# Kernel tuning notes

Hardware: AMD Instinct MI355X
Metric: run time of the kernel (lower is better)

Reference implementation:

```python
import jax, jax.numpy as jnp
import numpy as np

B, T, K, H = 8, 1024, 512, 8
MASKED = True

def setup_inputs() -> dict:
    key = jax.random.key(0)
    ks = jax.random.split(key, 6)
    s = 0.02
    return {
        "x": jax.random.normal(ks[0], (B, T, K), dtype=jnp.float32),
        "Wq": jax.random.normal(ks[1], (K, H * K), dtype=jnp.float32) * s,
        "Wk": jax.random.normal(ks[2], (K, H * K), dtype=jnp.float32) * s,
        "Wv": jax.random.normal(ks[3], (K, H * K), dtype=jnp.float32) * s,
        "Wu": jax.random.normal(ks[4], (H * K, K), dtype=jnp.float32) * s,
        "bu": jnp.zeros((K,), dtype=jnp.float32),
    }

def reference(x, Wq, Wk, Wv, Wu, bu):
    b, t, k = x.shape
    h = H
    scale = k ** (-0.25)  # applied to both q and k, as in the torch module
    q = (x @ Wq).reshape(b, t, h, k) * scale
    kk = (x @ Wk).reshape(b, t, h, k) * scale
    v = (x @ Wv).reshape(b, t, h, k)
    # scores: [b, h, t_q, t_k]
    dot = jnp.einsum("bthk,bshk->bhts", q, kk)
    if MASKED:
        causal = jnp.tril(jnp.ones((t, t), dtype=bool))
        dot = jnp.where(causal, dot, -jnp.inf)
    attn = jax.nn.softmax(dot, axis=-1)
    out = jnp.einsum("bhts,bshk->bthk", attn, v).reshape(b, t, h * k)
    return out @ Wu + bu
```

## Files before the change

kernel.cpp:

```cpp
#include <hip/hip_runtime.h>
#include <hip/hip_bf16.h>

#define T_SEQ 1024
#define NH 8
#define DH 512
#define HK 4096

typedef __attribute__((ext_vector_type(8))) __bf16 bf16x8;
typedef __attribute__((ext_vector_type(4))) float f32x4;

#define QK_SCALE 0.21022410381342863f
#define QK_SCALE_LOG2E 0.30328926584f

static __device__ __forceinline__ unsigned short f2bu(float f) {
  union { __hip_bfloat16 h; unsigned short u; } cv;
  cv.h = __float2bfloat16(f);
  return cv.u;
}

#define GLOAD_LDS16(gsrc, ldst) \
  __builtin_amdgcn_global_load_lds((const __attribute__((address_space(1))) void*)(gsrc), \
                                   (__attribute__((address_space(3))) void*)(ldst), 16, 0, 0)

__global__ void cvt_bf16_kernel(const float* __restrict__ in, unsigned short* __restrict__ out, int n4) {
  int i = blockIdx.x * blockDim.x + threadIdx.x;
  if (i >= n4) return;
  const float4 v = reinterpret_cast<const float4*>(in)[i];
  ushort4 u; u.x = f2bu(v.x); u.y = f2bu(v.y); u.z = f2bu(v.z); u.w = f2bu(v.w);
  reinterpret_cast<ushort4*>(out)[i] = u;
}

__global__ void transpose_cvt_kernel(const float* __restrict__ in, unsigned short* __restrict__ out,
                                     int R, int C) {
  __shared__ float tile[32][33];
  const int c0 = blockIdx.x * 32, r0 = blockIdx.y * 32;
  const int tx = threadIdx.x, ty = threadIdx.y;
  #pragma unroll
  for (int i = ty; i < 32; i += 8)
    tile[i][tx] = in[(size_t)(r0 + i) * C + (c0 + tx)];
  __syncthreads();
  #pragma unroll
  for (int i = ty; i < 32; i += 8)
    out[(size_t)(c0 + i) * R + (r0 + tx)] = f2bu(tile[tx][i]);
}

__global__ void transpose_cvt3_kernel(const float* __restrict__ Wq, const float* __restrict__ Wk,
                                      const float* __restrict__ Wv, unsigned short* __restrict__ out) {
  __shared__ float tile[32][33];
  const float* in = (blockIdx.z == 0) ? Wq : (blockIdx.z == 1) ? Wk : Wv;
  unsigned short* dst = out + (size_t)blockIdx.z * 4096 * 512;
  const int c0 = blockIdx.x * 32, r0 = blockIdx.y * 32;
  const int tx = threadIdx.x, ty = threadIdx.y;
  #pragma unroll
  for (int i = ty; i < 32; i += 8)
    tile[i][tx] = in[(size_t)(r0 + i) * 4096 + (c0 + tx)];
  __syncthreads();
  #pragma unroll
  for (int i = ty; i < 32; i += 8)
    dst[(size_t)(c0 + i) * 512 + (r0 + tx)] = f2bu(tile[tx][i]);
}

__global__ __launch_bounds__(256, 4)
void gemm_qkv(const unsigned short* __restrict__ A,
              const unsigned short* __restrict__ B,
              unsigned short* __restrict__ Qo,
              unsigned short* __restrict__ Ko,
              unsigned short* __restrict__ Vo) {
  __shared__ __align__(16) char smem[32768];
  char* As = smem;
  char* Bs = smem + 16384;
  const int tid = threadIdx.x, lane = tid & 63, w = tid >> 6;
  const int wr = w >> 1, wc = w & 1;
  const int bid = blockIdx.x;
  const int x = bid & 7, inner = bid >> 3;
  const int p0 = (x * 12 + inner % 12) * 128;
  const int p1 = (inner / 12) * 128;
  const int Kd = 512;

  f32x4 acc[4][4];
  #pragma unroll
  for (int i = 0; i < 4; ++i)
    #pragma unroll
    for (int j = 0; j < 4; ++j)
      acc[i][j] = f32x4{0.f, 0.f, 0.f, 0.f};

  for (int kt = 0; kt < Kd; kt += 64) {
    __syncthreads();
    #pragma unroll
    for (int is = 0; is < 4; ++is) {
      const int ob = is * 4096 + w * 1024;
      const int ol = ob + lane * 16;
      const int row = ol >> 7;
      const int bo = ol & 127;
      const int sw = (row & 7) << 4;
      GLOAD_LDS16((const char*)A + ((size_t)(p0 + row) * Kd + kt) * 2 + (bo ^ sw), As + ob);
      GLOAD_LDS16((const char*)B + ((size_t)(p1 + row) * Kd + kt) * 2 + (bo ^ sw), Bs + ob);
    }
    __syncthreads();
    #pragma unroll
    for (int ks = 0; ks < 2; ++ks) {
      bf16x8 af[4], bfr[4];
      #pragma unroll
      for (int mi = 0; mi < 4; ++mi) {
        const int row = wr * 64 + mi * 16 + (lane & 15);
        af[mi] = *reinterpret_cast<const bf16x8*>(
            As + row * 128 + ((ks * 64 + ((lane >> 4) << 4)) ^ ((row & 7) << 4)));
      }
      #pragma unroll
      for (int ni = 0; ni < 4; ++ni) {
        const int row = wc * 64 + ni * 16 + (lane & 15);
        bfr[ni] = *reinterpret_cast<const bf16x8*>(
            Bs + row * 128 + ((ks * 64 + ((lane >> 4) << 4)) ^ ((row & 7) << 4)));
      }
      #pragma unroll
      for (int mi = 0; mi < 4; ++mi)
        #pragma unroll
        for (int ni = 0; ni < 4; ++ni)
          acc[mi][ni] = __builtin_amdgcn_mfma_f32_16x16x32_bf16(af[mi], bfr[ni], acc[mi][ni], 0, 0, 0);
    }
  }

  const int region = p0 >> 12;
  if (region < 2) {
    const float qs = (region == 0) ? QK_SCALE_LOG2E : QK_SCALE;
    unsigned short* dst = (region == 0) ? Qo : Ko;
    #pragma unroll
    for (int mi = 0; mi < 4; ++mi) {
      #pragma unroll
      for (int ni = 0; ni < 4; ++ni) {
        const int n = p0 + wr * 64 + mi * 16 + ((lane >> 4) << 2);
        const int m = p1 + wc * 64 + ni * 16 + (lane & 15);
        const int b = m >> 10, t = m & 1023;
        const int nr = n & 4095, h = nr >> 9, d = nr & 511;
        ushort4 u;
        u.x = f2bu(acc[mi][ni][0] * qs); u.y = f2bu(acc[mi][ni][1] * qs);
        u.z = f2bu(acc[mi][ni][2] * qs); u.w = f2bu(acc[mi][ni][3] * qs);
        *reinterpret_cast<ushort4*>(&dst[((size_t)((b * NH + h) * T_SEQ + t)) * DH + d]) = u;
      }
    }
  } else {
    __syncthreads();
    unsigned short* Vl = reinterpret_cast<unsigned short*>(smem);
    const int key = (lane >> 4) << 3;
    #pragma unroll
    for (int mi = 0; mi < 4; ++mi) {
      #pragma unroll
      for (int ni = 0; ni < 4; ++ni) {
        const int dl = wr * 64 + mi * 16 + ((lane >> 4) << 2);
        const int tl = wc * 64 + ni * 16 + (lane & 15);
        #pragma unroll
        for (int r = 0; r < 4; ++r)
          Vl[(dl + r) * 128 + (tl ^ key)] = f2bu(acc[mi][ni][r]);
      }
    }
    __syncthreads();
    const int bb = p1 >> 10, t0 = p1 & 1023;
    const int hh = (p0 - 8192) >> 9, d0 = p0 & 511;
    unsigned short* vdst = Vo + ((size_t)(bb * NH + hh) * DH + d0) * T_SEQ + t0;
    #pragma unroll
    for (int i = 0; i < 8; ++i) {
      const int idx = i * 256 + tid;
      const int dr = idx >> 4, tc = (idx & 15) * 8;
      const int key2 = ((dr >> 2) & 3) << 3;
      *reinterpret_cast<uint4*>(vdst + (size_t)dr * T_SEQ + tc) =
          *reinterpret_cast<const uint4*>(Vl + dr * 128 + (tc ^ key2));
    }
  }
}

__global__ __launch_bounds__(256, 2)
void gemm_out(const unsigned short* __restrict__ A,
              const unsigned short* __restrict__ B,
              const float* __restrict__ bias,
              float* __restrict__ C) {
  __shared__ __align__(16) char As[2][8192];
  __shared__ __align__(16) char Bs[2][16384];
  const int tid = threadIdx.x, lane = tid & 63, w = tid >> 6;
  const int bid = blockIdx.x;
  const int cpx = gridDim.x >> 3;
  const int swz = (bid & 7) * cpx + (bid >> 3);
  const int c0 = (swz & 7) * 64;
  const int m0 = (swz >> 3) * 128;
  const int Kd = HK;

  f32x4 acc[4][2];
  #pragma unroll
  for (int i = 0; i < 4; ++i) {
    acc[i][0] = f32x4{0.f, 0.f, 0.f, 0.f};
    acc[i][1] = f32x4{0.f, 0.f, 0.f, 0.f};
  }

  auto stage = [&](int buf, int kt) {
    #pragma unroll
    for (int is = 0; is < 2; ++is) {
      const int ob = is * 4096 + w * 1024;
      const int ol = ob + lane * 16;
      const int row = ol >> 7;
      const int bo = ol & 127;
      const int sw = (row & 7) << 4;
      GLOAD_LDS16((const char*)A + ((size_t)(c0 + row) * Kd + kt) * 2 + (bo ^ sw), As[buf] + ob);
    }
    #pragma unroll
    for (int is = 0; is < 4; ++is) {
      const int ob = is * 4096 + w * 1024;
      const int ol = ob + lane * 16;
      const int row = ol >> 7;
      const int bo = ol & 127;
      const int sw = (row & 7) << 4;
      GLOAD_LDS16((const char*)B + ((size_t)(m0 + row) * Kd + kt) * 2 + (bo ^ sw), Bs[buf] + ob);
    }
  };

  stage(0, 0);
  __syncthreads();
  int cur = 0;
  for (int kt = 0; kt < Kd; kt += 64) {
    if (kt + 64 < Kd) stage(cur ^ 1, kt + 64);
    #pragma unroll
    for (int ks = 0; ks < 2; ++ks) {
      bf16x8 af[4], bfr[2];
      #pragma unroll
      for (int mi = 0; mi < 4; ++mi) {
        const int row = mi * 16 + (lane & 15);
        af[mi] = *reinterpret_cast<const bf16x8*>(
            As[cur] + row * 128 + ((ks * 64 + ((lane >> 4) << 4)) ^ ((row & 7) << 4)));
      }
      #pragma unroll
      for (int ni = 0; ni < 2; ++ni) {
        const int row = w * 32 + ni * 16 + (lane & 15);
        bfr[ni] = *reinterpret_cast<const bf16x8*>(
            Bs[cur] + row * 128 + ((ks * 64 + ((lane >> 4) << 4)) ^ ((row & 7) << 4)));
      }
      #pragma unroll
      for (int mi = 0; mi < 4; ++mi)
        #pragma unroll
        for (int ni = 0; ni < 2; ++ni)
          acc[mi][ni] = __builtin_amdgcn_mfma_f32_16x16x32_bf16(af[mi], bfr[ni], acc[mi][ni], 0, 0, 0);
    }
    __syncthreads();
    cur ^= 1;
  }

  #pragma unroll
  for (int mi = 0; mi < 4; ++mi) {
    const int c = c0 + mi * 16 + ((lane >> 4) << 2);
    const float4 bn = *reinterpret_cast<const float4*>(&bias[c]);
    #pragma unroll
    for (int ni = 0; ni < 2; ++ni) {
      const int m = m0 + w * 32 + ni * 16 + (lane & 15);
      float4 v;
      v.x = acc[mi][ni][0] + bn.x; v.y = acc[mi][ni][1] + bn.y;
      v.z = acc[mi][ni][2] + bn.z; v.w = acc[mi][ni][3] + bn.w;
      *reinterpret_cast<float4*>(&C[(size_t)m * DH + c]) = v;
    }
  }
}

__global__ __launch_bounds__(512, 1)
void attn_kernel(const unsigned short* __restrict__ Qg,
                 const unsigned short* __restrict__ Kg,
                 const unsigned short* __restrict__ Vtg,
                 unsigned short* __restrict__ Og) {
  __shared__ __align__(16) char Ks[2][32768];
  __shared__ __align__(16) char Vts[2][32768];
  __shared__ float S_lds[64 * 32];
  __shared__ __align__(16) char P_lds[64 * 64];
  __shared__ float Mrow[64], Lrow[64], Arow[64];
  __shared__ int rflag;

  const int tid = threadIdx.x, lane = tid & 63, w = tid >> 6;
  const int n = blockIdx.x;
  const int h = n & 7, p = (n >> 3) & 7, b = n >> 6;
  const int bh = b * NH + h;

  const unsigned short* Qbase = Qg + (size_t)bh * T_SEQ * DH;
  const char* Kbase = (const char*)(Kg + (size_t)bh * T_SEQ * DH);
  const char* Vbase = (const char*)(Vtg + (size_t)bh * DH * T_SEQ);

  auto stage = [&](int st, int buf) {
    #pragma unroll
    for (int is = 0; is < 4; ++is) {
      const int ob = is * 8192 + w * 1024;
      const int ol = ob + lane * 16;
      { const int row = ol >> 10, bo = ol & 1023;
        GLOAD_LDS16(Kbase + (size_t)(st * 32 + row) * 1024 + (bo ^ ((row & 7) << 4)), Ks[buf] + ob); }
      { const int row = ol >> 6, bo = ol & 63;
        GLOAD_LDS16(Vbase + (size_t)row * 2048 + st * 64 + (bo ^ ((row & 3) << 4)), Vts[buf] + ob); }
    }
  };

  for (int rep = 0; rep < 2; ++rep) {
    const int qt = rep ? 15 - p : p;
    const int nst = 2 * qt + 2;
    __syncthreads();

    bf16x8 qreg[16];
    {
      const int qrow = qt * 64 + ((w >> 1) << 4) + (lane & 15);
      const unsigned short* qp = Qbase + (size_t)qrow * DH + ((lane >> 4) << 3);
      #pragma unroll
      for (int k2 = 0; k2 < 16; ++k2)
        qreg[k2] = *reinterpret_cast<const bf16x8*>(qp + k2 * 32);
    }

    f32x4 o[2][8];
    #pragma unroll
    for (int mi = 0; mi < 2; ++mi)
      #pragma unroll
      for (int ni = 0; ni < 8; ++ni)
        o[mi][ni] = f32x4{0.f, 0.f, 0.f, 0.f};

    if (tid < 64) { Mrow[tid] = -INFINITY; Lrow[tid] = 0.f; }

    int cur = 0;
    stage(0, 0);

    for (int st = 0; st < nst; ++st) {
      __syncthreads();
      if (st + 1 < nst) stage(st + 1, cur ^ 1);
      if (tid == 0) rflag = 0;

      {
        const int krow = ((w & 1) << 4) + (lane & 15);
        const char* kr = Ks[cur] + krow * 1024;
        const int sw = (krow & 7) << 4;
        f32x4 s = f32x4{0.f, 0.f, 0.f, 0.f};
        __builtin_amdgcn_s_setprio(1);
        #pragma unroll
        for (int ks = 0; ks < 16; ++ks) {
          bf16x8 kf = *reinterpret_cast<const bf16x8*>(kr + ((ks * 64 + ((lane >> 4) << 4)) ^ sw));
          s = __builtin_amdgcn_mfma_f32_16x16x32_bf16(qreg[ks], kf, s, 0, 0, 0);
        }
        __builtin_amdgcn_s_setprio(0);
        const int col = ((w & 1) << 4) + (lane & 15);
        const int rbase = ((w >> 1) << 4) + ((lane >> 4) << 2);
        #pragma unroll
        for (int r = 0; r < 4; ++r)
          S_lds[(rbase + r) * 32 + (col ^ (((rbase + r) & 7) << 2))] = s[r];
      }
      asm volatile("s_waitcnt lgkmcnt(0)" ::: "memory");
      __builtin_amdgcn_sched_barrier(0);
      __builtin_amdgcn_s_barrier();

      {
        const int r = tid >> 3, cg = tid & 7;
        const int grow = qt * 64 + r;
        const int base = r * 32 + ((cg * 4) ^ ((r & 7) << 2));
        float sv[4];
        #pragma unroll
        for (int j = 0; j < 4; ++j) {
          const int c = cg * 4 + j;
          const float x = S_lds[base + j];
          sv[j] = (st * 32 + c > grow) ? -INFINITY : x;
        }
        float pm = fmaxf(fmaxf(sv[0], sv[1]), fmaxf(sv[2], sv[3]));
        pm = fmaxf(pm, __shfl_xor(pm, 1));
        pm = fmaxf(pm, __shfl_xor(pm, 2));
        pm = fmaxf(pm, __shfl_xor(pm, 4));
        const float m_old = Mrow[r];
        const bool defer = (pm <= m_old + 11.0f);
        const float m_new = defer ? m_old : pm;
        float ps;
        ushort4 pu;
        { float p0 = exp2f(sv[0] - m_new), p1 = exp2f(sv[1] - m_new),
                p2 = exp2f(sv[2] - m_new), p3 = exp2f(sv[3] - m_new);
          ps = p0 + p1 + p2 + p3;
          pu.x = f2bu(p0); pu.y = f2bu(p1); pu.z = f2bu(p2); pu.w = f2bu(p3); }
        *reinterpret_cast<ushort4*>(P_lds + r * 64 + ((cg * 8) ^ ((r & 3) << 4))) = pu;
        ps += __shfl_xor(ps, 1);
        ps += __shfl_xor(ps, 2);
        ps += __shfl_xor(ps, 4);
        if (cg == 0) {
          const float alpha = defer ? 1.0f : exp2f(m_old - m_new);
          if (!defer) { rflag = 1; Mrow[r] = m_new; }
          Arow[r] = alpha;
          Lrow[r] = alpha * Lrow[r] + ps;
        }
      }
      asm volatile("s_waitcnt lgkmcnt(0)" ::: "memory");
      __builtin_amdgcn_sched_barrier(0);
      __builtin_amdgcn_s_barrier();

      {
        bf16x8 pf[2];
        #pragma unroll
        for (int mi = 0; mi < 2; ++mi) {
          const int pr = ((w >> 2) << 5) + mi * 16 + (lane & 15);
          pf[mi] = *reinterpret_cast<const bf16x8*>(
              P_lds + pr * 64 + ((((lane >> 4) << 4)) ^ ((pr & 3) << 4)));
        }
        if (rflag) {
          #pragma unroll
          for (int mi = 0; mi < 2; ++mi) {
            const int rb = ((w >> 2) << 5) + mi * 16 + ((lane >> 4) << 2);
            const f32x4 al = f32x4{Arow[rb], Arow[rb + 1], Arow[rb + 2], Arow[rb + 3]};
            #pragma unroll
            for (int ni = 0; ni < 8; ++ni) o[mi][ni] *= al;
          }
        }
        __builtin_amdgcn_s_setprio(1);
        #pragma unroll
        for (int ni = 0; ni < 8; ++ni) {
          const int vr = ((w & 3) << 7) + ni * 16 + (lane & 15);
          bf16x8 vf = *reinterpret_cast<const bf16x8*>(
              Vts[cur] + vr * 64 + ((((lane >> 4) << 4)) ^ ((vr & 3) << 4)));
          o[0][ni] = __builtin_amdgcn_mfma_f32_16x16x32_bf16(pf[0], vf, o[0][ni], 0, 0, 0);
          o[1][ni] = __builtin_amdgcn_mfma_f32_16x16x32_bf16(pf[1], vf, o[1][ni], 0, 0, 0);
        }
        __builtin_amdgcn_s_setprio(0);
      }
      cur ^= 1;
    }

    #pragma unroll
    for (int mi = 0; mi < 2; ++mi) {
      const int rb = ((w >> 2) << 5) + mi * 16 + ((lane >> 4) << 2);
      f32x4 li;
      #pragma unroll
      for (int r = 0; r < 4; ++r) li[r] = 1.f / Lrow[rb + r];
      #pragma unroll
      for (int ni = 0; ni < 8; ++ni) {
        const int d = ((w & 3) << 7) + ni * 16 + (lane & 15);
        const size_t base = ((size_t)(b * T_SEQ + qt * 64 + rb) * NH + h) * DH + d;
        #pragma unroll
        for (int r = 0; r < 4; ++r)
          Og[base + (size_t)r * NH * DH] = f2bu(o[mi][ni][r] * li[r]);
      }
    }
  }
}

extern "C" void kernel_launch(void* const* d_in, const int* in_sizes, int n_in,
                              void* d_out, int out_size, void* d_ws, size_t ws_size,
                              hipStream_t stream) {
  (void)in_sizes; (void)n_in; (void)out_size;
  const float* x  = (const float*)d_in[0];
  const float* Wq = (const float*)d_in[1];
  const float* Wk = (const float*)d_in[2];
  const float* Wv = (const float*)d_in[3];
  const float* Wu = (const float*)d_in[4];
  const float* bu = (const float*)d_in[5];
  float* out = (float*)d_out;

  const size_t PERS = (size_t)8192 * 512 * 2 + 3 * (size_t)4096 * 512 * 2 + (size_t)512 * 4096 * 2;
  int NB = 8;
  while (NB > 1 && PERS + 4 * ((size_t)NB * 1024 * 4096 * 2) + 65536 > ws_size) NB >>= 1;

  size_t off = 0;
  auto wsp = [&](size_t bytes) {
    char* p = (char*)d_ws + off;
    off += (bytes + 255) & ~(size_t)255;
    return p;
  };
  unsigned short* xb   = (unsigned short*)wsp((size_t)8192 * 512 * 2);
  unsigned short* Wcat = (unsigned short*)wsp(3 * (size_t)4096 * 512 * 2);
  unsigned short* Wut  = (unsigned short*)wsp((size_t)512 * 4096 * 2);
  const size_t CHB = (size_t)NB * 1024 * 4096 * 2;
  unsigned short* Qc = (unsigned short*)wsp(CHB);
  unsigned short* Kc = (unsigned short*)wsp(CHB);
  unsigned short* Vc = (unsigned short*)wsp(CHB);
  unsigned short* Oc = (unsigned short*)wsp(CHB);

  cvt_bf16_kernel<<<4096, 256, 0, stream>>>(x, xb, 8192 * 512 / 4);
  transpose_cvt3_kernel<<<dim3(128, 16, 3), dim3(32, 8), 0, stream>>>(Wq, Wk, Wv, Wcat);
  transpose_cvt_kernel<<<dim3(16, 128), dim3(32, 8), 0, stream>>>(Wu, Wut, 4096, 512);

  const int nchunks = 8 / NB;
  for (int c = 0; c < nchunks; ++c) {
    const unsigned short* xc = xb + (size_t)c * NB * 1024 * 512;
    gemm_qkv<<<96 * NB * 8, 256, 0, stream>>>(Wcat, xc, Qc, Kc, Vc);
    attn_kernel<<<64 * NB, 512, 0, stream>>>(Qc, Kc, Vc, Oc);
    gemm_out<<<64 * NB, 256, 0, stream>>>(Wut, Oc, bu, out + (size_t)c * NB * 1024 * 512);
  }
}
```

Baseline: 445.4 us.

## Keep softmax in registers by computing transposed scores per wave

Restructures the attention inner loop so each wave computes S^T (K as A operand, Q as B) for its 16 query rows over all 32 keys, letting the row max/sum be done with cross-lane shuffles and the P fragment be built directly in registers for the PV MFMA. This removes the S_lds/P_lds round trips and two block-wide barriers per key step, and drops the shared M/L/alpha arrays. In exchange each wave redundantly computes both halves of the QK scores (pairs of waves share query rows), the V tile swizzle changes to allow split 8-byte reads, and each wave now holds 16 output accumulators instead of 2x8.

```diff
diff --git a/kernel.cpp b/kernel.cpp
--- a/kernel.cpp
+++ b/kernel.cpp
@@ -7,6 +7,7 @@
 #define HK 4096
 
 typedef __attribute__((ext_vector_type(8))) __bf16 bf16x8;
+typedef __attribute__((ext_vector_type(4))) __bf16 bf16x4;
 typedef __attribute__((ext_vector_type(4))) float f32x4;
 
 #define QK_SCALE 0.21022410381342863f
@@ -263,12 +264,9 @@
                  unsigned short* __restrict__ Og) {
   __shared__ __align__(16) char Ks[2][32768];
   __shared__ __align__(16) char Vts[2][32768];
-  __shared__ float S_lds[64 * 32];
-  __shared__ __align__(16) char P_lds[64 * 64];
-  __shared__ float Mrow[64], Lrow[64], Arow[64];
-  __shared__ int rflag;
 
   const int tid = threadIdx.x, lane = tid & 63, w = tid >> 6;
+  const int g = w >> 1, e = w & 1;
   const int n = blockIdx.x;
   const int h = n & 7, p = (n >> 3) & 7, b = n >> 6;
   const int bh = b * NH + h;
@@ -285,32 +283,31 @@
       { const int row = ol >> 10, bo = ol & 1023;
         GLOAD_LDS16(Kbase + (size_t)(st * 32 + row) * 1024 + (bo ^ ((row & 7) << 4)), Ks[buf] + ob); }
       { const int row = ol >> 6, bo = ol & 63;
-        GLOAD_LDS16(Vbase + (size_t)row * 2048 + st * 64 + (bo ^ ((row & 3) << 4)), Vts[buf] + ob); }
+        GLOAD_LDS16(Vbase + (size_t)row * 2048 + st * 64 + (bo ^ (((row >> 1) & 3) << 4)), Vts[buf] + ob); }
     }
   };
+
+  const int g8 = (lane >> 4) << 3;
 
   for (int rep = 0; rep < 2; ++rep) {
     const int qt = rep ? 15 - p : p;
     const int nst = 2 * qt + 2;
+    const int qglob = qt * 64 + g * 16 + (lane & 15);
     __syncthreads();
 
     bf16x8 qreg[16];
     {
-      const int qrow = qt * 64 + ((w >> 1) << 4) + (lane & 15);
-      const unsigned short* qp = Qbase + (size_t)qrow * DH + ((lane >> 4) << 3);
+      const unsigned short* qp = Qbase + (size_t)qglob * DH + g8;
       #pragma unroll
       for (int k2 = 0; k2 < 16; ++k2)
         qreg[k2] = *reinterpret_cast<const bf16x8*>(qp + k2 * 32);
     }
 
-    f32x4 o[2][8];
-    #pragma unroll
-    for (int mi = 0; mi < 2; ++mi)
-      #pragma unroll
-      for (int ni = 0; ni < 8; ++ni)
-        o[mi][ni] = f32x4{0.f, 0.f, 0.f, 0.f};
-
-    if (tid < 64) { Mrow[tid] = -INFINITY; Lrow[tid] = 0.f; }
+    f32x4 o[16];
+    #pragma unroll
+    for (int ni = 0; ni < 16; ++ni) o[ni] = f32x4{0.f, 0.f, 0.f, 0.f};
+
+    float M = -INFINITY, L = 0.f;
 
     int cur = 0;
     stage(0, 0);
@@ -318,113 +315,90 @@
     for (int st = 0; st < nst; ++st) {
       __syncthreads();
       if (st + 1 < nst) stage(st + 1, cur ^ 1);
-      if (tid == 0) rflag = 0;
-
+
+      f32x4 s0 = f32x4{0.f, 0.f, 0.f, 0.f}, s1 = s0;
       {
-        const int krow = ((w & 1) << 4) + (lane & 15);
-        const char* kr = Ks[cur] + krow * 1024;
-        const int sw = (krow & 7) << 4;
-        f32x4 s = f32x4{0.f, 0.f, 0.f, 0.f};
+        const int kr0 = lane & 15, kr1 = 16 + (lane & 15);
+        const char* ka = Ks[cur] + kr0 * 1024;
+        const char* kb = Ks[cur] + kr1 * 1024;
+        const int swa = (kr0 & 7) << 4, swb = (kr1 & 7) << 4;
         __builtin_amdgcn_s_setprio(1);
         #pragma unroll
-        for (int ks = 0; ks < 16; ++ks) {
-          bf16x8 kf = *reinterpret_cast<const bf16x8*>(kr + ((ks * 64 + ((lane >> 4) << 4)) ^ sw));
-          s = __builtin_amdgcn_mfma_f32_16x16x32_bf16(qreg[ks], kf, s, 0, 0, 0);
+        for (int kk = 0; kk < 16; ++kk) {
+          bf16x8 ra = *reinterpret_cast<const bf16x8*>(ka + ((kk * 64 + (g8 << 1)) ^ swa));
+          bf16x8 rb = *reinterpret_cast<const bf16x8*>(kb + ((kk * 64 + (g8 << 1)) ^ swb));
+          s0 = __builtin_amdgcn_mfma_f32_16x16x32_bf16(ra, qreg[kk], s0, 0, 0, 0);
+          s1 = __builtin_amdgcn_mfma_f32_16x16x32_bf16(rb, qreg[kk], s1, 0, 0, 0);
         }
         __builtin_amdgcn_s_setprio(0);
-        const int col = ((w & 1) << 4) + (lane & 15);
-        const int rbase = ((w >> 1) << 4) + ((lane >> 4) << 2);
-        #pragma unroll
-        for (int r = 0; r < 4; ++r)
-          S_lds[(rbase + r) * 32 + (col ^ (((rbase + r) & 7) << 2))] = s[r];
-      }
-      asm volatile("s_waitcnt lgkmcnt(0)" ::: "memory");
-      __builtin_amdgcn_sched_barrier(0);
-      __builtin_amdgcn_s_barrier();
+      }
 
       {
-        const int r = tid >> 3, cg = tid & 7;
-        const int grow = qt * 64 + r;
-        const int base = r * 32 + ((cg * 4) ^ ((r & 7) << 2));
-        float sv[4];
-        #pragma unroll
-        for (int j = 0; j < 4; ++j) {
-          const int c = cg * 4 + j;
-          const float x = S_lds[base + j];
-          sv[j] = (st * 32 + c > grow) ? -INFINITY : x;
+        const int kt0 = st * 32 + ((lane >> 4) << 2);
+        #pragma unroll
+        for (int r = 0; r < 4; ++r) {
+          if (kt0 + r > qglob)      s0[r] = -INFINITY;
+          if (kt0 + 16 + r > qglob) s1[r] = -INFINITY;
         }
-        float pm = fmaxf(fmaxf(sv[0], sv[1]), fmaxf(sv[2], sv[3]));
-        pm = fmaxf(pm, __shfl_xor(pm, 1));
-        pm = fmaxf(pm, __shfl_xor(pm, 2));
-        pm = fmaxf(pm, __shfl_xor(pm, 4));
-        const float m_old = Mrow[r];
-        const bool defer = (pm <= m_old + 11.0f);
-        const float m_new = defer ? m_old : pm;
-        float ps;
-        ushort4 pu;
-        { float p0 = exp2f(sv[0] - m_new), p1 = exp2f(sv[1] - m_new),
-                p2 = exp2f(sv[2] - m_new), p3 = exp2f(sv[3] - m_new);
-          ps = p0 + p1 + p2 + p3;
-          pu.x = f2bu(p0); pu.y = f2bu(p1); pu.z = f2bu(p2); pu.w = f2bu(p3); }
-        *reinterpret_cast<ushort4*>(P_lds + r * 64 + ((cg * 8) ^ ((r & 3) << 4))) = pu;
-        ps += __shfl_xor(ps, 1);
-        ps += __shfl_xor(ps, 2);
-        ps += __shfl_xor(ps, 4);
-        if (cg == 0) {
-          const float alpha = defer ? 1.0f : exp2f(m_old - m_new);
-          if (!defer) { rflag = 1; Mrow[r] = m_new; }
-          Arow[r] = alpha;
-          Lrow[r] = alpha * Lrow[r] + ps;
+        float pm = fmaxf(fmaxf(fmaxf(s0[0], s0[1]), fmaxf(s0[2], s0[3])),
+                         fmaxf(fmaxf(s1[0], s1[1]), fmaxf(s1[2], s1[3])));
+        pm = fmaxf(pm, __shfl_xor(pm, 16));
+        pm = fmaxf(pm, __shfl_xor(pm, 32));
+        const bool resc = (pm > M + 11.0f);
+        const float m_new = resc ? pm : M;
+        float p0[4], p1[4], ps = 0.f;
+        #pragma unroll
+        for (int r = 0; r < 4; ++r) { p0[r] = exp2f(s0[r] - m_new); ps += p0[r]; }
+        #pragma unroll
+        for (int r = 0; r < 4; ++r) { p1[r] = exp2f(s1[r] - m_new); ps += p1[r]; }
+        ps += __shfl_xor(ps, 16);
+        ps += __shfl_xor(ps, 32);
+        const float alpha = resc ? exp2f(M - m_new) : 1.0f;
+        M = m_new;
+        L = alpha * L + ps;
+
+        if (__ballot(resc)) {
+          f32x4 al;
+          #pragma unroll
+          for (int r = 0; r < 4; ++r)
+            al[r] = __shfl(alpha, ((lane >> 4) << 2) + r);
+          #pragma unroll
+          for (int ni = 0; ni < 16; ++ni) o[ni] *= al;
         }
-      }
-      asm volatile("s_waitcnt lgkmcnt(0)" ::: "memory");
-      __builtin_amdgcn_sched_barrier(0);
-      __builtin_amdgcn_s_barrier();
-
-      {
-        bf16x8 pf[2];
-        #pragma unroll
-        for (int mi = 0; mi < 2; ++mi) {
-          const int pr = ((w >> 2) << 5) + mi * 16 + (lane & 15);
-          pf[mi] = *reinterpret_cast<const bf16x8*>(
-              P_lds + pr * 64 + ((((lane >> 4) << 4)) ^ ((pr & 3) << 4)));
-        }
-        if (rflag) {
-          #pragma unroll
-          for (int mi = 0; mi < 2; ++mi) {
-            const int rb = ((w >> 2) << 5) + mi * 16 + ((lane >> 4) << 2);
-            const f32x4 al = f32x4{Arow[rb], Arow[rb + 1], Arow[rb + 2], Arow[rb + 3]};
-            #pragma unroll
-            for (int ni = 0; ni < 8; ++ni) o[mi][ni] *= al;
-          }
-        }
+
+        bf16x4 pa0 = {(__bf16)p0[0], (__bf16)p0[1], (__bf16)p0[2], (__bf16)p0[3]};
+        bf16x4 pa1 = {(__bf16)p1[0], (__bf16)p1[1], (__bf16)p1[2], (__bf16)p1[3]};
+        bf16x8 pa = __builtin_shufflevector(pa0, pa1, 0, 1, 2, 3, 4, 5, 6, 7);
+
         __builtin_amdgcn_s_setprio(1);
         #pragma unroll
-        for (int ni = 0; ni < 8; ++ni) {
-          const int vr = ((w & 3) << 7) + ni * 16 + (lane & 15);
-          bf16x8 vf = *reinterpret_cast<const bf16x8*>(
-              Vts[cur] + vr * 64 + ((((lane >> 4) << 4)) ^ ((vr & 3) << 4)));
-          o[0][ni] = __builtin_amdgcn_mfma_f32_16x16x32_bf16(pf[0], vf, o[0][ni], 0, 0, 0);
-          o[1][ni] = __builtin_amdgcn_mfma_f32_16x16x32_bf16(pf[1], vf, o[1][ni], 0, 0, 0);
+        for (int ni = 0; ni < 16; ++ni) {
+          const int vr = (e << 8) + ni * 16 + (lane & 15);
+          const char* vrow = Vts[cur] + vr * 64;
+          const int sw = ((vr >> 1) & 3) << 4;
+          bf16x4 vlo = *reinterpret_cast<const bf16x4*>(vrow + (g8 ^ sw));
+          bf16x4 vhi = *reinterpret_cast<const bf16x4*>(vrow + ((32 + g8) ^ sw));
+          bf16x8 vf = __builtin_shufflevector(vlo, vhi, 0, 1, 2, 3, 4, 5, 6, 7);
+          o[ni] = __builtin_amdgcn_mfma_f32_16x16x32_bf16(pa, vf, o[ni], 0, 0, 0);
         }
         __builtin_amdgcn_s_setprio(0);
       }
       cur ^= 1;
     }
 
-    #pragma unroll
-    for (int mi = 0; mi < 2; ++mi) {
-      const int rb = ((w >> 2) << 5) + mi * 16 + ((lane >> 4) << 2);
+    {
       f32x4 li;
       #pragma unroll
-      for (int r = 0; r < 4; ++r) li[r] = 1.f / Lrow[rb + r];
-      #pragma unroll
-      for (int ni = 0; ni < 8; ++ni) {
-        const int d = ((w & 3) << 7) + ni * 16 + (lane & 15);
-        const size_t base = ((size_t)(b * T_SEQ + qt * 64 + rb) * NH + h) * DH + d;
+      for (int r = 0; r < 4; ++r)
+        li[r] = 1.0f / __shfl(L, ((lane >> 4) << 2) + r);
+      const int trow = qt * 64 + g * 16 + ((lane >> 4) << 2);
+      #pragma unroll
+      for (int ni = 0; ni < 16; ++ni) {
+        const int d = (e << 8) + ni * 16 + (lane & 15);
+        const size_t base = ((size_t)(b * T_SEQ + trow) * NH + h) * DH + d;
         #pragma unroll
         for (int r = 0; r < 4; ++r)
-          Og[base + (size_t)r * NH * DH] = f2bu(o[mi][ni][r] * li[r]);
+          Og[base + (size_t)r * NH * DH] = f2bu(o[ni][r] * li[r]);
       }
     }
   }
```

Result: slower. 491.7 us (+10.4%).

## Shrink output GEMM tiles and drop double buffering for more blocks

Applied to the files above, without the earlier changes.

The output projection GEMM moves from 64x128 tiles with a double-buffered K=64 pipeline to 32x64 tiles with a single buffer over K=128 steps. The grid is four times larger, launch bounds allow 4 blocks per CU, and the XCD-aware block mapping is rewritten so each XCD gets contiguous M tiles. The aim is more parallelism and occupancy for a GEMM that launched few blocks. The cost is lower arithmetic intensity per tile, more global traffic from re-reading operands, and load latency that is no longer overlapped with compute inside a block.

```diff
diff --git a/kernel.cpp b/kernel.cpp
--- a/kernel.cpp
+++ b/kernel.cpp
@@ -168,91 +168,66 @@
   }
 }
 
-__global__ __launch_bounds__(256, 2)
+__global__ __launch_bounds__(256, 4)
 void gemm_out(const unsigned short* __restrict__ A,
               const unsigned short* __restrict__ B,
               const float* __restrict__ bias,
               float* __restrict__ C) {
-  __shared__ __align__(16) char As[2][8192];
-  __shared__ __align__(16) char Bs[2][16384];
+  __shared__ __align__(16) char As[8192];
+  __shared__ __align__(16) char Bs[16384];
   const int tid = threadIdx.x, lane = tid & 63, w = tid >> 6;
   const int bid = blockIdx.x;
-  const int cpx = gridDim.x >> 3;
-  const int swz = (bid & 7) * cpx + (bid >> 3);
-  const int c0 = (swz & 7) * 64;
-  const int m0 = (swz >> 3) * 128;
+  const int x = bid & 7, inner = bid >> 3;
+  const int mtiles_per_xcd = gridDim.x >> 7;
+  const int c0 = (inner & 15) * 32;
+  const int m0 = (x * mtiles_per_xcd + (inner >> 4)) * 64;
   const int Kd = HK;
 
-  f32x4 acc[4][2];
-  #pragma unroll
-  for (int i = 0; i < 4; ++i) {
-    acc[i][0] = f32x4{0.f, 0.f, 0.f, 0.f};
-    acc[i][1] = f32x4{0.f, 0.f, 0.f, 0.f};
-  }
-
-  auto stage = [&](int buf, int kt) {
+  f32x4 acc[2];
+  acc[0] = f32x4{0.f, 0.f, 0.f, 0.f};
+  acc[1] = f32x4{0.f, 0.f, 0.f, 0.f};
+
+  for (int kt = 0; kt < Kd; kt += 128) {
+    __syncthreads();
     #pragma unroll
     for (int is = 0; is < 2; ++is) {
       const int ob = is * 4096 + w * 1024;
       const int ol = ob + lane * 16;
-      const int row = ol >> 7;
-      const int bo = ol & 127;
-      const int sw = (row & 7) << 4;
-      GLOAD_LDS16((const char*)A + ((size_t)(c0 + row) * Kd + kt) * 2 + (bo ^ sw), As[buf] + ob);
+      const int row = ol >> 8, bo = ol & 255;
+      GLOAD_LDS16((const char*)A + ((size_t)(c0 + row) * Kd + kt) * 2 + (bo ^ ((row & 15) << 4)), As + ob);
     }
     #pragma unroll
     for (int is = 0; is < 4; ++is) {
       const int ob = is * 4096 + w * 1024;
       const int ol = ob + lane * 16;
-      const int row = ol >> 7;
-      const int bo = ol & 127;
-      const int sw = (row & 7) << 4;
-      GLOAD_LDS16((const char*)B + ((size_t)(m0 + row) * Kd + kt) * 2 + (bo ^ sw), Bs[buf] + ob);
-    }
-  };
-
-  stage(0, 0);
-  __syncthreads();
-  int cur = 0;
-  for (int kt = 0; kt < Kd; kt += 64) {
-    if (kt + 64 < Kd) stage(cur ^ 1, kt + 64);
-    #pragma unroll
-    for (int ks = 0; ks < 2; ++ks) {
-      bf16x8 af[4], bfr[2];
-      #pragma unroll
-      for (int mi = 0; mi < 4; ++mi) {
-        const int row = mi * 16 + (lane & 15);
-        af[mi] = *reinterpret_cast<const bf16x8*>(
-            As[cur] + row * 128 + ((ks * 64 + ((lane >> 4) << 4)) ^ ((row & 7) << 4)));
-      }
-      #pragma unroll
-      for (int ni = 0; ni < 2; ++ni) {
-        const int row = w * 32 + ni * 16 + (lane & 15);
-        bfr[ni] = *reinterpret_cast<const bf16x8*>(
-            Bs[cur] + row * 128 + ((ks * 64 + ((lane >> 4) << 4)) ^ ((row & 7) << 4)));
-      }
-      #pragma unroll
-      for (int mi = 0; mi < 4; ++mi)
-        #pragma unroll
-        for (int ni = 0; ni < 2; ++ni)
-          acc[mi][ni] = __builtin_amdgcn_mfma_f32_16x16x32_bf16(af[mi], bfr[ni], acc[mi][ni], 0, 0, 0);
-    }
-    __syncthreads();
-    cur ^= 1;
-  }
-
-  #pragma unroll
-  for (int mi = 0; mi < 4; ++mi) {
-    const int c = c0 + mi * 16 + ((lane >> 4) << 2);
+      const int row = ol >> 8, bo = ol & 255;
+      GLOAD_LDS16((const char*)B + ((size_t)(m0 + row) * Kd + kt) * 2 + (bo ^ ((row & 15) << 4)), Bs + ob);
+    }
+    __syncthreads();
+    #pragma unroll
+    for (int ks = 0; ks < 4; ++ks) {
+      const int ko = ks * 64 + ((lane >> 4) << 4);
+      bf16x8 af0, af1, bf;
+      { const int row = (lane & 15);
+        af0 = *reinterpret_cast<const bf16x8*>(As + row * 256 + (ko ^ ((row & 15) << 4))); }
+      { const int row = 16 + (lane & 15);
+        af1 = *reinterpret_cast<const bf16x8*>(As + row * 256 + (ko ^ ((row & 15) << 4))); }
+      { const int row = w * 16 + (lane & 15);
+        bf = *reinterpret_cast<const bf16x8*>(Bs + row * 256 + (ko ^ ((row & 15) << 4))); }
+      acc[0] = __builtin_amdgcn_mfma_f32_16x16x32_bf16(af0, bf, acc[0], 0, 0, 0);
+      acc[1] = __builtin_amdgcn_mfma_f32_16x16x32_bf16(af1, bf, acc[1], 0, 0, 0);
+    }
+  }
+
+  const int m = m0 + w * 16 + (lane & 15);
+  #pragma unroll
+  for (int fc = 0; fc < 2; ++fc) {
+    const int c = c0 + fc * 16 + ((lane >> 4) << 2);
     const float4 bn = *reinterpret_cast<const float4*>(&bias[c]);
-    #pragma unroll
-    for (int ni = 0; ni < 2; ++ni) {
-      const int m = m0 + w * 32 + ni * 16 + (lane & 15);
-      float4 v;
-      v.x = acc[mi][ni][0] + bn.x; v.y = acc[mi][ni][1] + bn.y;
-      v.z = acc[mi][ni][2] + bn.z; v.w = acc[mi][ni][3] + bn.w;
-      *reinterpret_cast<float4*>(&C[(size_t)m * DH + c]) = v;
-    }
+    float4 v;
+    v.x = acc[fc][0] + bn.x; v.y = acc[fc][1] + bn.y;
+    v.z = acc[fc][2] + bn.z; v.w = acc[fc][3] + bn.w;
+    *reinterpret_cast<float4*>(&C[(size_t)m * DH + c]) = v;
   }
 }
 
@@ -470,6 +445,6 @@
     const unsigned short* xc = xb + (size_t)c * NB * 1024 * 512;
     gemm_qkv<<<96 * NB * 8, 256, 0, stream>>>(Wcat, xc, Qc, Kc, Vc);
     attn_kernel<<<64 * NB, 512, 0, stream>>>(Qc, Kc, Vc, Oc);
-    gemm_out<<<64 * NB, 256, 0, stream>>>(Wut, Oc, bu, out + (size_t)c * NB * 1024 * 512);
-  }
-}
+    gemm_out<<<256 * NB, 256, 0, stream>>>(Wut, Oc, bu, out + (size_t)c * NB * 1024 * 512);
+  }
+}
```

Result: faster. 421.2 us (-5.4%).
